# Performance work log

Measured on AMD Instinct MI355X. Metric: run time of the kernel, lower is better.

The kernel has to match this reference:

```python
import jax, jax.numpy as jnp
import numpy as np

B, S, D, H = 2, 2048, 768, 12
HD = D // H  # head_dim = 64


def setup_inputs() -> dict:
    key = jax.random.key(0)
    ks = jax.random.split(key, 9)
    s = 1.0 / np.sqrt(D)
    return {
        "x": jax.random.normal(ks[0], (B, S, D), dtype=jnp.float32),
        "Wq": jax.random.normal(ks[1], (D, D), dtype=jnp.float32) * s,
        "bq": jnp.zeros((D,), dtype=jnp.float32),
        "Wk": jax.random.normal(ks[2], (D, D), dtype=jnp.float32) * s,
        "bk": jnp.zeros((D,), dtype=jnp.float32),
        "Wv": jax.random.normal(ks[3], (D, D), dtype=jnp.float32) * s,
        "bv": jnp.zeros((D,), dtype=jnp.float32),
        "Wo": jax.random.normal(ks[4], (D, D), dtype=jnp.float32) * s,
        "bo": jnpp if False else jnp.zeros((D,), dtype=jnp.float32),
    }


def reference(x, Wq, bq, Wk, bk, Wv, bv, Wo, bo):
    b, s, d = x.shape
    # projections, split heads: [b, h, s, hd]
    def proj(W, bias):
        y = x @ W + bias
        return y.reshape(b, s, H, HD).transpose(0, 2, 1, 3)

    q = proj(Wq, bq)
    k = proj(Wk, bk)
    v = proj(Wv, bv)

    scale = 1.0 / jnp.sqrt(jnp.float32(HD))
    scores = jnp.einsum("bhqd,bhkd->bhqk", q, k) * scale
    causal = jnp.tril(jnp.ones((s, s), dtype=bool))  # True where allowed
    scores = jnp.where(causal, scores, -jnp.inf)
    attn = jax.nn.softmax(scores, axis=-1)
    ctx = jnp.einsum("bhqk,bhkd->bhqd", attn, v)
    ctx = ctx.transpose(0, 2, 1, 3).reshape(b, s, d)
    return ctx @ Wo + bo
```

## Files before the change

kernel.cpp:

```cpp
#include <hip/hip_runtime.h>
#include <stdint.h>

typedef unsigned short u16;
typedef __attribute__((ext_vector_type(8))) short s16x8;
typedef __attribute__((ext_vector_type(4))) float f32x4;
typedef __attribute__((ext_vector_type(16))) float f32x16;

#define MFMA_BF16(a, b, c) __builtin_amdgcn_mfma_f32_16x16x32_bf16((a), (b), (c), 0, 0, 0)
#define MFMA32(a, b, c) __builtin_amdgcn_mfma_f32_32x32x16_bf16((a), (b), (c), 0, 0, 0)

typedef const __attribute__((address_space(1))) uint32_t* gas1_t;
typedef __attribute__((address_space(3))) uint32_t* las3_t;
#define GLDS16(dst, src) __builtin_amdgcn_global_load_lds((gas1_t)(src), (las3_t)(dst), 16, 0, 0)

static __device__ __forceinline__ u16 f2bf(float f) {
    uint32_t u = __float_as_uint(f);
    u = (u + 0x7fffu + ((u >> 16) & 1u)) >> 16;
    return (u16)u;
}
static __device__ __forceinline__ uint32_t pk2bf(float a, float b) {
    return (uint32_t)f2bf(a) | ((uint32_t)f2bf(b) << 16);
}

__global__ void k_cvt_bf16(const float* __restrict__ in, u16* __restrict__ out) {
    int i = (blockIdx.x * 256 + threadIdx.x) * 8;
    f32x4 a = *(const f32x4*)(in + i);
    f32x4 b = *(const f32x4*)(in + i + 4);
    s16x8 r;
    r[0] = (short)f2bf(a[0]); r[1] = (short)f2bf(a[1]);
    r[2] = (short)f2bf(a[2]); r[3] = (short)f2bf(a[3]);
    r[4] = (short)f2bf(b[0]); r[5] = (short)f2bf(b[1]);
    r[6] = (short)f2bf(b[2]); r[7] = (short)f2bf(b[3]);
    *(s16x8*)(out + i) = r;
}

__global__ void k_transpose_w(const float* __restrict__ w0, const float* __restrict__ w1,
                              const float* __restrict__ w2, const float* __restrict__ w3,
                              u16* __restrict__ t0, u16* __restrict__ t1,
                              u16* __restrict__ t2, u16* __restrict__ t3) {
    __shared__ float tile[32][33];
    const float* W; u16* T;
    switch (blockIdx.z) {
        case 0:  W = w0; T = t0; break;
        case 1:  W = w1; T = t1; break;
        case 2:  W = w2; T = t2; break;
        default: W = w3; T = t3; break;
    }
    int n0 = blockIdx.x * 32, k0 = blockIdx.y * 32;
    int tx = threadIdx.x, ty = threadIdx.y;
#pragma unroll
    for (int i = 0; i < 4; ++i)
        tile[ty + 8 * i][tx] = W[(size_t)(k0 + ty + 8 * i) * 768 + n0 + tx];
    __syncthreads();
#pragma unroll
    for (int i = 0; i < 4; ++i)
        T[(size_t)(n0 + ty + 8 * i) * 768 + k0 + tx] = f2bf(tile[tx][ty + 8 * i]);
}

template <int MODE>
__global__ __launch_bounds__(256) void k_gemm128(
        const u16* __restrict__ A,
        const u16* __restrict__ btq, const u16* __restrict__ btk, const u16* __restrict__ btv,
        const float* __restrict__ bq, const float* __restrict__ bk, const float* __restrict__ bv,
        u16* __restrict__ outq, u16* __restrict__ outk, u16* __restrict__ outv,
        float* __restrict__ outf) {
    __shared__ __align__(16) char ldsb[32768];
    u16* lA = (u16*)ldsb;
    u16* lB = (u16*)(ldsb + 16384);
    int sel, nb;
    const u16* Bt; const float* bias;
    if (MODE == 0) {
        sel = blockIdx.x / 6; nb = blockIdx.x % 6;
        if (sel == 0)      { Bt = btq; bias = bq; }
        else if (sel == 1) { Bt = btk; bias = bk; }
        else               { Bt = btv; bias = bv; }
    } else {
        sel = 0; nb = blockIdx.x; Bt = btq; bias = bq;
    }
    const int t = threadIdx.x, lane = t & 63, w = t >> 6;
    const int wr = w >> 1, wc = w & 1;
    const int c = lane & 15, g = lane >> 4;
    const int m0 = blockIdx.y * 128, n0 = nb * 128;
    f32x4 acc[4][4] = {};
    const int srow = 8 * w + (lane >> 3);
    const int scol = 8 * ((lane & 7) ^ ((lane >> 3) & 7));
    const u16* gA = A  + (size_t)(m0 + srow) * 768 + scol;
    const u16* gB = Bt + (size_t)(n0 + srow) * 768 + scol;
    for (int kb = 0; kb < 768; kb += 64) {
#pragma unroll
        for (int j = 0; j < 4; ++j) {
            GLDS16(&lA[j * 2048 + w * 512], gA + (size_t)j * 32 * 768 + kb);
            GLDS16(&lB[j * 2048 + w * 512], gB + (size_t)j * 32 * 768 + kb);
        }
        __syncthreads();
#pragma unroll
        for (int kh = 0; kh < 2; ++kh) {
            s16x8 af[4], bf[4];
            const int gg = kh * 4 + g;
#pragma unroll
            for (int i = 0; i < 4; ++i) {
                int ra = wr * 64 + i * 16 + c;
                af[i] = *(const s16x8*)&lA[ra * 64 + 8 * (gg ^ (ra & 7))];
                int rb = wc * 64 + i * 16 + c;
                bf[i] = *(const s16x8*)&lB[rb * 64 + 8 * (gg ^ (rb & 7))];
            }
#pragma unroll
            for (int i = 0; i < 4; ++i)
#pragma unroll
                for (int j = 0; j < 4; ++j)
                    acc[i][j] = MFMA_BF16(af[i], bf[j], acc[i][j]);
        }
        __syncthreads();
    }
    const float C2 = 0.18033688011112042f;
    float* lC = (float*)ldsb;
    const float osc = (MODE == 0 && sel == 0) ? C2 : 1.0f;
#pragma unroll
    for (int j4 = 0; j4 < 4; ++j4) {
        if (wc == (j4 >> 1)) {
#pragma unroll
            for (int jj = 0; jj < 2; ++jj) {
                const int j = (j4 & 1) * 2 + jj;
                const int n = n0 + wc * 64 + j * 16 + c;
                const float bvv = bias[n];
                const int colb = (j * 16 + c) & 31;
#pragma unroll
                for (int i = 0; i < 4; ++i)
#pragma unroll
                    for (int rr = 0; rr < 4; ++rr) {
                        const int m = wr * 64 + i * 16 + g * 4 + rr;
                        const float v = (acc[i][j][rr] + bvv) * osc;
                        if (MODE == 0 && sel == 2) lC[colb * 130 + m] = v;
                        else                       lC[m * 34 + colb] = v;
                    }
            }
        }
        __syncthreads();
        if (MODE == 1) {
#pragma unroll
            for (int it = 0; it < 2; ++it) {
                const int p = t + it * 256, sl = p >> 2, cb = (p & 3) * 8;
                f32x4 v0, v1;
#pragma unroll
                for (int e = 0; e < 4; ++e) { v0[e] = lC[sl * 34 + cb + e]; v1[e] = lC[sl * 34 + cb + 4 + e]; }
                float* op = outf + (size_t)(m0 + sl) * 768 + n0 + j4 * 32 + cb;
                *(f32x4*)op = v0; *(f32x4*)(op + 4) = v1;
            }
        } else if (sel < 2) {
            u16* outp = (sel == 0) ? outq : outk;
#pragma unroll
            for (int it = 0; it < 2; ++it) {
                const int p = t + it * 256, sl = p >> 2, cb = (p & 3) * 8;
                s16x8 ov;
#pragma unroll
                for (int e = 0; e < 8; ++e) ov[e] = (short)f2bf(lC[sl * 34 + cb + e]);
                const int ng = n0 + j4 * 32 + cb, hh = ng >> 6, hd = ng & 63;
                const int m = m0 + sl, bb = m >> 11, ss = m & 2047;
                *(s16x8*)&outp[(((size_t)(bb * 12 + hh) * 2048 + ss) << 6) + hd] = ov;
            }
        } else {
#pragma unroll
            for (int it = 0; it < 2; ++it) {
                const int p = t + it * 256, nn = p >> 4, mb = (p & 15) * 8;
                s16x8 ov;
#pragma unroll
                for (int e = 0; e < 8; ++e) ov[e] = (short)f2bf(lC[nn * 130 + mb + e]);
                const int ng = n0 + j4 * 32 + nn, hh = ng >> 6, hd = ng & 63;
                const int bb = m0 >> 11, ss = (m0 & 2047) + mb;
                *(s16x8*)&outv[((size_t)(bb * 12 + hh) * 64 + hd) * 2048 + ss] = ov;
            }
        }
        __syncthreads();
    }
}

__global__ __launch_bounds__(256) void k_attn(const u16* __restrict__ qw,
                                              const u16* __restrict__ kw,
                                              const u16* __restrict__ vt,
                                              u16* __restrict__ ctxb) {
    __shared__ u16 lK[2][64 * 64];
    __shared__ u16 lV[2][64 * 64];
    const int bid = blockIdx.x;
    const int qt = 15 - bid / 24;
    const int bh = bid % 24;
    const int t = threadIdx.x, lane = t & 63, w = t >> 6;
    const int l31 = lane & 31, hi = lane >> 5;
    const int q0w = qt * 128 + w * 32;
    const u16* qp = qw + (size_t)bh * 2048 * 64;
    const u16* kp = kw + (size_t)bh * 2048 * 64;
    const u16* vp = vt + (size_t)bh * 64 * 2048;
    s16x8 qf[4];
#pragma unroll
    for (int dk = 0; dk < 4; ++dk)
        qf[dk] = *(const s16x8*)&qp[(size_t)(q0w + l31) * 64 + dk * 16 + hi * 8];
    asm volatile("s_waitcnt vmcnt(0)" ::: "memory");
    const int lr = lane >> 3, lg = lane & 7;
    const int swz8 = 8 * (lg ^ lr);
    const u16* kpb = kp + (size_t)(w * 16 + lr) * 64 + swz8;
    const u16* vpb = vp + (size_t)(w * 16 + lr) * 2048 + swz8;
    const int NC = 2 * qt + 2;
    const int lastq = q0w + 31;
    f32x16 ct[2] = {};
    float m2 = -1e30f, ssum = 0.0f;
#define STAGE(bf, ch)                                                          \
    {                                                                          \
        const u16* ks_ = kpb + (size_t)(ch) * 4096;                            \
        GLDS16(&lK[bf][(w * 16) * 64], ks_);                                   \
        GLDS16(&lK[bf][(w * 16 + 8) * 64], ks_ + 512);                         \
        const u16* vs_ = vpb + (size_t)(ch) * 64;                              \
        GLDS16(&lV[bf][(w * 16) * 64], vs_);                                   \
        GLDS16(&lV[bf][(w * 16 + 8) * 64], vs_ + 8 * 2048);                    \
    }
    STAGE(0, 0);
    for (int ch = 0; ch < NC; ++ch) {
        const int bf = ch & 1, Kc = ch * 64;
        if (ch + 1 < NC) {
            STAGE(bf ^ 1, ch + 1);
            asm volatile("s_waitcnt vmcnt(4)" ::: "memory");
        } else {
            asm volatile("s_waitcnt vmcnt(0)" ::: "memory");
        }
        __builtin_amdgcn_sched_barrier(0);
        __builtin_amdgcn_s_barrier();
        if (Kc <= lastq) {
            f32x16 st[2] = {};
#pragma unroll
            for (int dk = 0; dk < 4; ++dk) {
                const int gr = dk * 2 + hi;
                const int r0 = l31, r1 = 32 + l31;
                s16x8 kf0 = *(const s16x8*)&lK[bf][r0 * 64 + 8 * (gr ^ (r0 & 7))];
                s16x8 kf1 = *(const s16x8*)&lK[bf][r1 * 64 + 8 * (gr ^ (r1 & 7))];
                st[0] = MFMA32(kf0, qf[dk], st[0]);
                st[1] = MFMA32(kf1, qf[dk], st[1]);
            }
            const int qg = q0w + l31;
            float tv[32];
            if (Kc + 63 <= q0w) {
#pragma unroll
                for (int j = 0; j < 16; ++j) { tv[j] = st[0][j]; tv[16 + j] = st[1][j]; }
            } else {
                const int kb = Kc + 4 * hi;
#pragma unroll
                for (int j = 0; j < 16; ++j) {
                    const int kloc = (j & 3) + 8 * (j >> 2);
                    tv[j]      = (kb + kloc      <= qg) ? st[0][j] : -1e30f;
                    tv[16 + j] = (kb + kloc + 32 <= qg) ? st[1][j] : -1e30f;
                }
            }
            float mt = tv[0];
#pragma unroll
            for (int j = 1; j < 32; ++j) mt = fmaxf(mt, tv[j]);
            if (!__all(mt <= m2 + 8.0f)) {
                float mq = fmaxf(mt, __shfl_xor(mt, 32));
                const float mnew = fmaxf(m2, mq);
                const float fac = __builtin_amdgcn_exp2f(m2 - mnew);
                ssum *= fac;
#pragma unroll
                for (int j = 0; j < 16; ++j) { ct[0][j] *= fac; ct[1][j] *= fac; }
                m2 = mnew;
            }
            float p[32];
#pragma unroll
            for (int j = 0; j < 32; ++j) { p[j] = __builtin_amdgcn_exp2f(tv[j] - m2); ssum += p[j]; }
#pragma unroll
            for (int kt = 0; kt < 2; ++kt) {
                uint32_t pcv[8];
#pragma unroll
                for (int x = 0; x < 8; ++x) {
                    const int j = kt * 16 + 4 * (x >> 1) + 2 * (x & 1);
                    asm volatile("v_cvt_pk_bf16_f32 %0, %1, %2"
                                 : "=v"(pcv[x]) : "v"(p[j]), "v"(p[j + 1]));
                }
#pragma unroll
                for (int kl = 0; kl < 2; ++kl) {
                    const uint32_t s0 = hi ? pcv[4 * kl]     : pcv[4 * kl + 2];
                    const uint32_t s1 = hi ? pcv[4 * kl + 1] : pcv[4 * kl + 3];
                    const uint32_t r0 = __shfl_xor(s0, 32);
                    const uint32_t r1 = __shfl_xor(s1, 32);
                    union { uint32_t u[4]; s16x8 v; } pf;
                    pf.u[0] = hi ? r0 : pcv[4 * kl];
                    pf.u[1] = hi ? r1 : pcv[4 * kl + 1];
                    pf.u[2] = hi ? pcv[4 * kl + 2] : r0;
                    pf.u[3] = hi ? pcv[4 * kl + 3] : r1;
                    const int gr = (kt * 2 + kl) * 2 + hi;
                    const int rv0 = l31, rv1 = 32 + l31;
                    s16x8 vf0 = *(const s16x8*)&lV[bf][rv0 * 64 + 8 * (gr ^ (rv0 & 7))];
                    s16x8 vf1 = *(const s16x8*)&lV[bf][rv1 * 64 + 8 * (gr ^ (rv1 & 7))];
                    ct[0] = MFMA32(vf0, pf.v, ct[0]);
                    ct[1] = MFMA32(vf1, pf.v, ct[1]);
                }
            }
        }
        __builtin_amdgcn_s_barrier();
    }
    ssum += __shfl_xor(ssum, 32);
    const float inv = 1.0f / ssum;
    const int b = bh / 12, h = bh - b * 12;
    const size_t base = (size_t)(b * 2048 + q0w + l31) * 768 + h * 64;
#pragma unroll
    for (int ht = 0; ht < 2; ++ht)
#pragma unroll
        for (int a = 0; a < 4; ++a) {
            const int hd = ht * 32 + 8 * a + 4 * hi;
            uint64_t pk = (uint64_t)pk2bf(ct[ht][4 * a] * inv, ct[ht][4 * a + 1] * inv) |
                          ((uint64_t)pk2bf(ct[ht][4 * a + 2] * inv, ct[ht][4 * a + 3] * inv) << 32);
            *(uint64_t*)&ctxb[base + hd] = pk;
        }
#undef STAGE
}

extern "C" void kernel_launch(void* const* d_in, const int* in_sizes, int n_in,
                              void* d_out, int out_size, void* d_ws, size_t ws_size,
                              hipStream_t stream) {
    (void)in_sizes; (void)n_in; (void)out_size; (void)ws_size;
    const float* x  = (const float*)d_in[0];
    const float* Wq = (const float*)d_in[1];
    const float* bq = (const float*)d_in[2];
    const float* Wk = (const float*)d_in[3];
    const float* bk = (const float*)d_in[4];
    const float* Wv = (const float*)d_in[5];
    const float* bv = (const float*)d_in[6];
    const float* Wo = (const float*)d_in[7];
    const float* bo = (const float*)d_in[8];
    char* ws = (char*)d_ws;
    u16* xb   = (u16*)(ws);
    u16* wqt  = (u16*)(ws + 6291456);
    u16* wkt  = (u16*)(ws + 7471104);
    u16* wvt  = (u16*)(ws + 8650752);
    u16* wot  = (u16*)(ws + 9830400);
    u16* qwv  = (u16*)(ws + 11010048);
    u16* kwv  = (u16*)(ws + 17301504);
    u16* vtw  = (u16*)(ws + 23592960);
    u16* ctx  = (u16*)(ws + 29884416);
    float* out = (float*)d_out;

    k_cvt_bf16<<<1536, 256, 0, stream>>>(x, xb);
    k_transpose_w<<<dim3(24, 24, 4), dim3(32, 8), 0, stream>>>(Wq, Wk, Wv, Wo, wqt, wkt, wvt, wot);
    k_gemm128<0><<<dim3(18, 32), 256, 0, stream>>>(xb, wqt, wkt, wvt, bq, bk, bv,
                                                   qwv, kwv, vtw, nullptr);
    k_attn<<<384, 256, 0, stream>>>(qwv, kwv, vtw, ctx);
    k_gemm128<1><<<dim3(6, 32), 256, 0, stream>>>(ctx, wot, nullptr, nullptr, bo, nullptr, nullptr,
                                                  nullptr, nullptr, nullptr, out);
}
```

Before: 199.1 us.

## Shrink GEMM and attention tiles to raise grid size and drop LDS epilogues

The QKV projection now uses 128x64 tiles that map one block to one head, and the output GEMM uses a separate 64x64-tile kernel. Both write results directly from registers instead of staging them through LDS. Attention moves to 128-thread blocks with 64 query rows each, giving twice as many blocks, and adds s_setprio around the MFMA sections. More blocks improve occupancy and load balance across CUs, but smaller tiles mean less data reuse and the direct writes are less coalesced.

Measured after the change: 172.6 us. 13.3% less time.

```diff
diff --git a/kernel.cpp b/kernel.cpp
--- a/kernel.cpp
+++ b/kernel.cpp
@@ -57,135 +57,163 @@
         T[(size_t)(n0 + ty + 8 * i) * 768 + k0 + tx] = f2bf(tile[tx][ty + 8 * i]);
 }
 
-template <int MODE>
-__global__ __launch_bounds__(256) void k_gemm128(
+__global__ __launch_bounds__(256) void k_gemm_qkv(
         const u16* __restrict__ A,
         const u16* __restrict__ btq, const u16* __restrict__ btk, const u16* __restrict__ btv,
         const float* __restrict__ bq, const float* __restrict__ bk, const float* __restrict__ bv,
-        u16* __restrict__ outq, u16* __restrict__ outk, u16* __restrict__ outv,
-        float* __restrict__ outf) {
-    __shared__ __align__(16) char ldsb[32768];
-    u16* lA = (u16*)ldsb;
-    u16* lB = (u16*)(ldsb + 16384);
-    int sel, nb;
+        u16* __restrict__ outq, u16* __restrict__ outk, u16* __restrict__ outv) {
+    __shared__ u16 lA[128 * 64];
+    __shared__ u16 lB[64 * 64];
+    const int bx = blockIdx.x, sel = bx / 12, nb = bx - sel * 12;
     const u16* Bt; const float* bias;
-    if (MODE == 0) {
-        sel = blockIdx.x / 6; nb = blockIdx.x % 6;
-        if (sel == 0)      { Bt = btq; bias = bq; }
-        else if (sel == 1) { Bt = btk; bias = bk; }
-        else               { Bt = btv; bias = bv; }
-    } else {
-        sel = 0; nb = blockIdx.x; Bt = btq; bias = bq;
-    }
+    if (sel == 0)      { Bt = btq; bias = bq; }
+    else if (sel == 1) { Bt = btk; bias = bk; }
+    else               { Bt = btv; bias = bv; }
     const int t = threadIdx.x, lane = t & 63, w = t >> 6;
     const int wr = w >> 1, wc = w & 1;
     const int c = lane & 15, g = lane >> 4;
-    const int m0 = blockIdx.y * 128, n0 = nb * 128;
-    f32x4 acc[4][4] = {};
-    const int srow = 8 * w + (lane >> 3);
-    const int scol = 8 * ((lane & 7) ^ ((lane >> 3) & 7));
-    const u16* gA = A  + (size_t)(m0 + srow) * 768 + scol;
-    const u16* gB = Bt + (size_t)(n0 + srow) * 768 + scol;
+    const int m0 = blockIdx.y * 128, n0 = nb * 64;
+    f32x4 acc[4][2] = {};
+    const int lr = lane >> 3, lg = lane & 7;
+    const int swz8 = 8 * (lg ^ lr);
+    const u16* gA = A  + (size_t)(m0 + w * 8 + lr) * 768 + swz8;
+    const u16* gB = Bt + (size_t)(n0 + w * 8 + lr) * 768 + swz8;
     for (int kb = 0; kb < 768; kb += 64) {
 #pragma unroll
-        for (int j = 0; j < 4; ++j) {
+        for (int j = 0; j < 4; ++j)
             GLDS16(&lA[j * 2048 + w * 512], gA + (size_t)j * 32 * 768 + kb);
+#pragma unroll
+        for (int j = 0; j < 2; ++j)
             GLDS16(&lB[j * 2048 + w * 512], gB + (size_t)j * 32 * 768 + kb);
-        }
         __syncthreads();
 #pragma unroll
         for (int kh = 0; kh < 2; ++kh) {
-            s16x8 af[4], bf[4];
+            s16x8 af[4], bfr[2];
             const int gg = kh * 4 + g;
 #pragma unroll
             for (int i = 0; i < 4; ++i) {
-                int ra = wr * 64 + i * 16 + c;
+                const int ra = wr * 64 + i * 16 + c;
                 af[i] = *(const s16x8*)&lA[ra * 64 + 8 * (gg ^ (ra & 7))];
-                int rb = wc * 64 + i * 16 + c;
-                bf[i] = *(const s16x8*)&lB[rb * 64 + 8 * (gg ^ (rb & 7))];
+            }
+#pragma unroll
+            for (int j = 0; j < 2; ++j) {
+                const int rb = wc * 32 + j * 16 + c;
+                bfr[j] = *(const s16x8*)&lB[rb * 64 + 8 * (gg ^ (rb & 7))];
             }
 #pragma unroll
             for (int i = 0; i < 4; ++i)
 #pragma unroll
-                for (int j = 0; j < 4; ++j)
+                for (int j = 0; j < 2; ++j)
+                    acc[i][j] = MFMA_BF16(af[i], bfr[j], acc[i][j]);
+        }
+        __syncthreads();
+    }
+    const float C2 = 0.18033688011112042f;
+    const int h = nb;
+    if (sel < 2) {
+        u16* outp = (sel == 0) ? outq : outk;
+        const float osc = (sel == 0) ? C2 : 1.0f;
+#pragma unroll
+        for (int i = 0; i < 4; ++i)
+#pragma unroll
+            for (int j = 0; j < 2; ++j) {
+                const int hd = wc * 32 + j * 16 + c;
+                const float bvv = bias[n0 + hd];
+#pragma unroll
+                for (int rr = 0; rr < 4; ++rr) {
+                    const int m = m0 + wr * 64 + i * 16 + g * 4 + rr;
+                    const int b = m >> 11, s = m & 2047;
+                    outp[(((size_t)(b * 12 + h) * 2048 + s) << 6) + hd] =
+                        f2bf((acc[i][j][rr] + bvv) * osc);
+                }
+            }
+    } else {
+#pragma unroll
+        for (int i = 0; i < 4; ++i)
+#pragma unroll
+            for (int j = 0; j < 2; ++j) {
+                const int hd = wc * 32 + j * 16 + c;
+                const float bvv = bias[n0 + hd];
+                const int m = m0 + wr * 64 + i * 16 + g * 4;
+                const int b = m >> 11, s = m & 2047;
+                uint64_t pk = (uint64_t)pk2bf(acc[i][j][0] + bvv, acc[i][j][1] + bvv) |
+                              ((uint64_t)pk2bf(acc[i][j][2] + bvv, acc[i][j][3] + bvv) << 32);
+                *(uint64_t*)&outv[((size_t)(b * 12 + h) * 64 + hd) * 2048 + s] = pk;
+            }
+    }
+}
+
+__global__ __launch_bounds__(256) void k_gemm_out(const u16* __restrict__ A,
+                                                  const u16* __restrict__ Bt,
+                                                  const float* __restrict__ bias,
+                                                  float* __restrict__ out) {
+    __shared__ u16 lA[64 * 64];
+    __shared__ u16 lB[64 * 64];
+    const int t = threadIdx.x;
+    const int lane = t & 63, w = t >> 6;
+    const int wr = w >> 1, wc = w & 1;
+    const int c = lane & 15, g = lane >> 4;
+    const int m0 = blockIdx.y * 64, n0 = blockIdx.x * 64;
+    f32x4 acc[2][2] = {};
+    const int lr = lane >> 3, lq = lane & 7;
+    const int sq = (lq ^ lr) * 8;
+    const u16* gA0 = A  + (size_t)(m0 + w * 16 + lr) * 768 + sq;
+    const u16* gA1 = gA0 + 8 * 768;
+    const u16* gB0 = Bt + (size_t)(n0 + w * 16 + lr) * 768 + sq;
+    const u16* gB1 = gB0 + 8 * 768;
+    u16* dA0 = &lA[w * 1024];
+    u16* dA1 = &lA[w * 1024 + 512];
+    u16* dB0 = &lB[w * 1024];
+    u16* dB1 = &lB[w * 1024 + 512];
+    for (int kb = 0; kb < 768; kb += 64) {
+        GLDS16(dA0, gA0 + kb); GLDS16(dA1, gA1 + kb);
+        GLDS16(dB0, gB0 + kb); GLDS16(dB1, gB1 + kb);
+        __syncthreads();
+#pragma unroll
+        for (int st = 0; st < 2; ++st) {
+            s16x8 af[2], bf[2];
+            const int col = st * 32 + g * 8;
+#pragma unroll
+            for (int i = 0; i < 2; ++i) {
+                int ra = wr * 32 + i * 16 + c;
+                af[i] = *(const s16x8*)&lA[ra * 64 + (col ^ ((ra & 7) << 3))];
+                int rb = wc * 32 + i * 16 + c;
+                bf[i] = *(const s16x8*)&lB[rb * 64 + (col ^ ((rb & 7) << 3))];
+            }
+#pragma unroll
+            for (int i = 0; i < 2; ++i)
+#pragma unroll
+                for (int j = 0; j < 2; ++j)
                     acc[i][j] = MFMA_BF16(af[i], bf[j], acc[i][j]);
         }
         __syncthreads();
     }
-    const float C2 = 0.18033688011112042f;
-    float* lC = (float*)ldsb;
-    const float osc = (MODE == 0 && sel == 0) ? C2 : 1.0f;
-#pragma unroll
-    for (int j4 = 0; j4 < 4; ++j4) {
-        if (wc == (j4 >> 1)) {
-#pragma unroll
-            for (int jj = 0; jj < 2; ++jj) {
-                const int j = (j4 & 1) * 2 + jj;
-                const int n = n0 + wc * 64 + j * 16 + c;
-                const float bvv = bias[n];
-                const int colb = (j * 16 + c) & 31;
-#pragma unroll
-                for (int i = 0; i < 4; ++i)
-#pragma unroll
-                    for (int rr = 0; rr < 4; ++rr) {
-                        const int m = wr * 64 + i * 16 + g * 4 + rr;
-                        const float v = (acc[i][j][rr] + bvv) * osc;
-                        if (MODE == 0 && sel == 2) lC[colb * 130 + m] = v;
-                        else                       lC[m * 34 + colb] = v;
-                    }
-            }
-        }
-        __syncthreads();
-        if (MODE == 1) {
-#pragma unroll
-            for (int it = 0; it < 2; ++it) {
-                const int p = t + it * 256, sl = p >> 2, cb = (p & 3) * 8;
-                f32x4 v0, v1;
-#pragma unroll
-                for (int e = 0; e < 4; ++e) { v0[e] = lC[sl * 34 + cb + e]; v1[e] = lC[sl * 34 + cb + 4 + e]; }
-                float* op = outf + (size_t)(m0 + sl) * 768 + n0 + j4 * 32 + cb;
-                *(f32x4*)op = v0; *(f32x4*)(op + 4) = v1;
-            }
-        } else if (sel < 2) {
-            u16* outp = (sel == 0) ? outq : outk;
-#pragma unroll
-            for (int it = 0; it < 2; ++it) {
-                const int p = t + it * 256, sl = p >> 2, cb = (p & 3) * 8;
-                s16x8 ov;
-#pragma unroll
-                for (int e = 0; e < 8; ++e) ov[e] = (short)f2bf(lC[sl * 34 + cb + e]);
-                const int ng = n0 + j4 * 32 + cb, hh = ng >> 6, hd = ng & 63;
-                const int m = m0 + sl, bb = m >> 11, ss = m & 2047;
-                *(s16x8*)&outp[(((size_t)(bb * 12 + hh) * 2048 + ss) << 6) + hd] = ov;
-            }
-        } else {
-#pragma unroll
-            for (int it = 0; it < 2; ++it) {
-                const int p = t + it * 256, nn = p >> 4, mb = (p & 15) * 8;
-                s16x8 ov;
-#pragma unroll
-                for (int e = 0; e < 8; ++e) ov[e] = (short)f2bf(lC[nn * 130 + mb + e]);
-                const int ng = n0 + j4 * 32 + nn, hh = ng >> 6, hd = ng & 63;
-                const int bb = m0 >> 11, ss = (m0 & 2047) + mb;
-                *(s16x8*)&outv[((size_t)(bb * 12 + hh) * 64 + hd) * 2048 + ss] = ov;
-            }
-        }
-        __syncthreads();
-    }
-}
-
-__global__ __launch_bounds__(256) void k_attn(const u16* __restrict__ qw,
+#pragma unroll
+    for (int i = 0; i < 2; ++i)
+#pragma unroll
+        for (int j = 0; j < 2; ++j) {
+            const int n = n0 + wc * 32 + j * 16 + c;
+            const float bvv = bias[n];
+#pragma unroll
+            for (int rr = 0; rr < 4; ++rr) {
+                const int m = m0 + wr * 32 + i * 16 + g * 4 + rr;
+                out[(size_t)m * 768 + n] = acc[i][j][rr] + bvv;
+            }
+        }
+}
+
+__global__ __launch_bounds__(128) void k_attn(const u16* __restrict__ qw,
                                               const u16* __restrict__ kw,
                                               const u16* __restrict__ vt,
                                               u16* __restrict__ ctxb) {
     __shared__ u16 lK[2][64 * 64];
     __shared__ u16 lV[2][64 * 64];
     const int bid = blockIdx.x;
-    const int qt = 15 - bid / 24;
+    const int qt = 31 - bid / 24;
     const int bh = bid % 24;
     const int t = threadIdx.x, lane = t & 63, w = t >> 6;
     const int l31 = lane & 31, hi = lane >> 5;
-    const int q0w = qt * 128 + w * 32;
+    const int q0w = qt * 64 + w * 32;
     const u16* qp = qw + (size_t)bh * 2048 * 64;
     const u16* kp = kw + (size_t)bh * 2048 * 64;
     const u16* vp = vt + (size_t)bh * 64 * 2048;
@@ -196,34 +224,39 @@
     asm volatile("s_waitcnt vmcnt(0)" ::: "memory");
     const int lr = lane >> 3, lg = lane & 7;
     const int swz8 = 8 * (lg ^ lr);
-    const u16* kpb = kp + (size_t)(w * 16 + lr) * 64 + swz8;
-    const u16* vpb = vp + (size_t)(w * 16 + lr) * 2048 + swz8;
-    const int NC = 2 * qt + 2;
+    const u16* kpb = kp + (size_t)(w * 8 + lr) * 64 + swz8;
+    const u16* vpb = vp + (size_t)(w * 8 + lr) * 2048 + swz8;
+    const int NC = qt + 1;
     const int lastq = q0w + 31;
     f32x16 ct[2] = {};
     float m2 = -1e30f, ssum = 0.0f;
 #define STAGE(bf, ch)                                                          \
     {                                                                          \
         const u16* ks_ = kpb + (size_t)(ch) * 4096;                            \
-        GLDS16(&lK[bf][(w * 16) * 64], ks_);                                   \
-        GLDS16(&lK[bf][(w * 16 + 8) * 64], ks_ + 512);                         \
+        GLDS16(&lK[bf][(w * 8) * 64], ks_);                                    \
+        GLDS16(&lK[bf][(16 + w * 8) * 64], ks_ + 16 * 64);                     \
+        GLDS16(&lK[bf][(32 + w * 8) * 64], ks_ + 32 * 64);                     \
+        GLDS16(&lK[bf][(48 + w * 8) * 64], ks_ + 48 * 64);                     \
         const u16* vs_ = vpb + (size_t)(ch) * 64;                              \
-        GLDS16(&lV[bf][(w * 16) * 64], vs_);                                   \
-        GLDS16(&lV[bf][(w * 16 + 8) * 64], vs_ + 8 * 2048);                    \
+        GLDS16(&lV[bf][(w * 8) * 64], vs_);                                    \
+        GLDS16(&lV[bf][(16 + w * 8) * 64], vs_ + 16 * 2048);                   \
+        GLDS16(&lV[bf][(32 + w * 8) * 64], vs_ + 32 * 2048);                   \
+        GLDS16(&lV[bf][(48 + w * 8) * 64], vs_ + 48 * 2048);                   \
     }
     STAGE(0, 0);
     for (int ch = 0; ch < NC; ++ch) {
         const int bf = ch & 1, Kc = ch * 64;
         if (ch + 1 < NC) {
             STAGE(bf ^ 1, ch + 1);
-            asm volatile("s_waitcnt vmcnt(4)" ::: "memory");
+            asm volatile("s_waitcnt vmcnt(8)" ::: "memory");
         } else {
             asm volatile("s_waitcnt vmcnt(0)" ::: "memory");
         }
         __builtin_amdgcn_sched_barrier(0);
         __builtin_amdgcn_s_barrier();
-        if (Kc <= lastq) {
+        {
             f32x16 st[2] = {};
+            __builtin_amdgcn_s_setprio(1);
 #pragma unroll
             for (int dk = 0; dk < 4; ++dk) {
                 const int gr = dk * 2 + hi;
@@ -233,6 +266,7 @@
                 st[0] = MFMA32(kf0, qf[dk], st[0]);
                 st[1] = MFMA32(kf1, qf[dk], st[1]);
             }
+            __builtin_amdgcn_s_setprio(0);
             const int qg = q0w + l31;
             float tv[32];
             if (Kc + 63 <= q0w) {
@@ -286,8 +320,10 @@
                     const int rv0 = l31, rv1 = 32 + l31;
                     s16x8 vf0 = *(const s16x8*)&lV[bf][rv0 * 64 + 8 * (gr ^ (rv0 & 7))];
                     s16x8 vf1 = *(const s16x8*)&lV[bf][rv1 * 64 + 8 * (gr ^ (rv1 & 7))];
+                    __builtin_amdgcn_s_setprio(1);
                     ct[0] = MFMA32(vf0, pf.v, ct[0]);
                     ct[1] = MFMA32(vf1, pf.v, ct[1]);
+                    __builtin_amdgcn_s_setprio(0);
                 }
             }
         }
@@ -336,9 +372,7 @@
 
     k_cvt_bf16<<<1536, 256, 0, stream>>>(x, xb);
     k_transpose_w<<<dim3(24, 24, 4), dim3(32, 8), 0, stream>>>(Wq, Wk, Wv, Wo, wqt, wkt, wvt, wot);
-    k_gemm128<0><<<dim3(18, 32), 256, 0, stream>>>(xb, wqt, wkt, wvt, bq, bk, bv,
-                                                   qwv, kwv, vtw, nullptr);
-    k_attn<<<384, 256, 0, stream>>>(qwv, kwv, vtw, ctx);
-    k_gemm128<1><<<dim3(6, 32), 256, 0, stream>>>(ctx, wot, nullptr, nullptr, bo, nullptr, nullptr,
-                                                  nullptr, nullptr, nullptr, out);
-}
+    k_gemm_qkv<<<dim3(36, 32), 256, 0, stream>>>(xb, wqt, wkt, wvt, bq, bk, bv, qwv, kwv, vtw);
+    k_attn<<<768, 128, 0, stream>>>(qwv, kwv, vtw, ctx);
+    k_gemm_out<<<dim3(12, 64), 256, 0, stream>>>(ctx, wot, bo, out);
+}
```
